# Performance work log

Measured on AMD Instinct MI355X. Metric: run time of the kernel, lower is better.

## Reference

```python
import jax, jax.numpy as jnp
import numpy as np

WS = 10                      # window radius
K = 2 * WS + 1               # 21
K2 = K * K                   # 441 window positions
SIG_COLOR = 1.0 / (0.1 * 0.1 * 2.0)
SIG_SPACE = 1.0 / (7.0 * 7.0 * 2.0)
LP = 0.8
C1 = 10.0
C2 = 5.0
ALPHA = 5.0
EPS = 1e-6


def _patches(img):
    """torch nn.Unfold(kernel_size=image_size, padding=WS) trick: returns the
    K2 zero-padded shifted copies of the image, shape (b, K2, c, h, w)."""
    b, c, h, w = img.shape
    p = jax.lax.conv_general_dilated_patches(img, (K, K), (1, 1), [(WS, WS), (WS, WS)])
    # (b, c*K2, h, w) with channel-major (c, ky, kx) ordering -> (b, K2, c, h, w)
    return p.reshape(b, c, K2, h, w).transpose(0, 2, 1, 3, 4)


def _edge_response(img):
    # local contrast: sum over window and channels of |I_j - I_i| (zero-padded
    # / non-positive neighbors masked out), shape (b, h, w)
    p = _patches(img)
    d = jnp.where(p > 0, p - img[:, None], 0.0)
    return jnp.abs(d).sum(axis=(1, 2))


def setup_inputs() -> dict:
    key = jax.random.key(0)
    k1, k2 = jax.random.split(key)
    original_images = jax.random.uniform(k1, (1, 3, 224, 224), dtype=jnp.float32)
    smooth_images = jax.random.uniform(k2, (1, 3, 224, 224), dtype=jnp.float32)
    return {"original_images": original_images, "smooth_images": smooth_images}


def reference(original_images, smooth_images):
    b, c, h, w = smooth_images.shape

    # ti_minus_tj: |T_j - T_i| with zero/non-positive padded neighbors zeroed;
    # the shifted copies are detached in the original (stop_gradient)
    sp = jax.lax.stop_gradient(_patches(smooth_images))
    ti = jnp.abs(jnp.where(sp > 0, sp - smooth_images[:, None], 0.0))  # (b,K2,c,h,w)

    # edge-response based region masks
    er_o = _edge_response(original_images)
    er_s = _edge_response(smooth_images)
    use_large = ((er_o < C1) & (er_s - er_o > C2))[:, None, None]  # (b,1,1,h,w)

    # spatial affinity ws (constant gaussian over window offsets)
    dy = jnp.arange(-WS, WS + 1)
    ws = jnp.exp(-SIG_SPACE * (dy[:, None] ** 2 + dy[None, :] ** 2).astype(jnp.float32))
    ws = ws.reshape(1, K2, 1, 1, 1)

    # color affinity wr from the guidance (original) image; note the original
    # code computes the affinity BEFORE masking the color difference, so the
    # affinity includes zero-padded neighbors -- replicated faithfully
    op = jax.lax.stop_gradient(_patches(original_images))
    cd = ((op - original_images[:, None]) ** 2).sum(axis=2, keepdims=True)  # (b,K2,1,h,w)
    wr = jnp.exp(-SIG_COLOR * cd)

    ws = jnp.where(use_large, ws, 0.0)
    wr = jnp.where(~use_large, wr, 0.0)

    scale = 1.0 / (h * w * b) / (WS * WS)  # note: window_size**2, not K2 (quirk kept)
    return scale * jnp.sum(ALPHA * ws * ti ** 2 + wr * (ti + EPS) ** LP)
```

## Files before the change

### kernel.cpp

```cpp
#include <hip/hip_runtime.h>


#define WSR 10
#define KK  21
#define HH  224
#define WW  224
#define HWSZ (HH*WW)
#define SIG_COLOR 50.0f
#define SIG_SPACE (1.0f/98.0f)
#define LPW 0.8f
#define C1T 10.0f
#define C2T 5.0f
#define ALPHA_W 5.0f
#define EPSV 1e-6f
#define LOG2E 1.44269504088896f

__device__ __forceinline__ float fexp2(float x) { return __builtin_amdgcn_exp2f(x); }
__device__ __forceinline__ float flog2(float x) { return __builtin_amdgcn_logf(x); }
__device__ __forceinline__ float fexpe(float x) { return fexp2(x * LOG2E); }

__global__ __launch_bounds__(256) void smooth_loss_main(
    const float* __restrict__ orig, const float* __restrict__ smo,
    float* __restrict__ partials)
{
    __shared__ float w1[KK];
    __shared__ float racc[4][256];

    const int tid = threadIdx.x;
    if (tid < KK) {
        float d = (float)(tid - WSR);
        w1[tid] = fexpe(-SIG_SPACE * d * d);
    }
    __syncthreads();

    const int lane = tid & 63;
    const int wv   = tid >> 6;
    const int pix  = blockIdx.x * 64 + lane;
    const int py   = pix / WW;
    const int px   = pix - py * WW;

    const float oc0 = orig[pix], oc1 = orig[pix + HWSZ], oc2 = orig[pix + 2*HWSZ];
    const float sc0 = smo[pix],  sc1 = smo[pix + HWSZ],  sc2 = smo[pix + 2*HWSZ];

    const int ky0 = (wv == 0) ? 0 : (5 * wv + 1);
    const int kyn = (wv == 0) ? 6 : 5;

    float er_o = 0.f, er_s = 0.f, sl = 0.f, ss = 0.f;

    for (int kyi = 0; kyi < kyn; ++kyi) {
        const int ky = ky0 + kyi;
        const int y  = py + ky - WSR;
        const bool yv = ((unsigned)y < (unsigned)HH);
        const float wy = w1[ky];
        const int rb = y * WW;
        #pragma unroll 7
        for (int kx = 0; kx < KK; ++kx) {
            const int x = px + kx - WSR;
            const bool v = yv & ((unsigned)x < (unsigned)WW);
            const int ni = rb + x;
            float o0 = 0.f, o1 = 0.f, o2 = 0.f;
            float s0 = 0.f, s1 = 0.f, s2 = 0.f;
            if (v) {
                o0 = orig[ni]; o1 = orig[ni + HWSZ]; o2 = orig[ni + 2*HWSZ];
                s0 = smo[ni];  s1 = smo[ni + HWSZ];  s2 = smo[ni + 2*HWSZ];
            }
            float d0 = (o0 > 0.f) ? (o0 - oc0) : 0.f;
            float d1 = (o1 > 0.f) ? (o1 - oc1) : 0.f;
            float d2 = (o2 > 0.f) ? (o2 - oc2) : 0.f;
            er_o += fabsf(d0) + fabsf(d1) + fabsf(d2);
            float t0 = (s0 > 0.f) ? fabsf(s0 - sc0) : 0.f;
            float t1 = (s1 > 0.f) ? fabsf(s1 - sc1) : 0.f;
            float t2 = (s2 > 0.f) ? fabsf(s2 - sc2) : 0.f;
            er_s += t0 + t1 + t2;
            float e0 = o0 - oc0, e1 = o1 - oc1, e2 = o2 - oc2;
            float wr = fexpe(-SIG_COLOR * (e0*e0 + e1*e1 + e2*e2));
            float wsp = wy * w1[kx];
            sl += wsp * (t0*t0 + t1*t1 + t2*t2);
            float p0 = fexp2(LPW * flog2(t0 + EPSV));
            float p1 = fexp2(LPW * flog2(t1 + EPSV));
            float p2 = fexp2(LPW * flog2(t2 + EPSV));
            ss += wr * (p0 + p1 + p2);
        }
    }

    racc[0][tid] = er_o; racc[1][tid] = er_s;
    racc[2][tid] = sl;   racc[3][tid] = ss;
    __syncthreads();

    if (wv == 0) {
        float eo = racc[0][lane] + racc[0][64+lane] + racc[0][128+lane] + racc[0][192+lane];
        float es = racc[1][lane] + racc[1][64+lane] + racc[1][128+lane] + racc[1][192+lane];
        float l  = racc[2][lane] + racc[2][64+lane] + racc[2][128+lane] + racc[2][192+lane];
        float s  = racc[3][lane] + racc[3][64+lane] + racc[3][128+lane] + racc[3][192+lane];
        const bool use_large = (eo < C1T) && ((es - eo) > C2T);
        float contrib = use_large ? (ALPHA_W * l) : s;
        #pragma unroll
        for (int off = 32; off > 0; off >>= 1)
            contrib += __shfl_down(contrib, off, 64);
        if (lane == 0) partials[blockIdx.x] = contrib;
    }
}

__global__ __launch_bounds__(256) void smooth_loss_reduce(
    const float* __restrict__ partials, float* __restrict__ out, int n)
{
    __shared__ float red[256];
    const int tid = threadIdx.x;
    float v = 0.f;
    for (int i = tid; i < n; i += 256) v += partials[i];
    red[tid] = v;
    __syncthreads();
    if (tid < 128) red[tid] += red[tid + 128];
    __syncthreads();
    if (tid < 64) {
        float x = red[tid] + red[tid + 64];
        #pragma unroll
        for (int off = 32; off > 0; off >>= 1)
            x += __shfl_down(x, off, 64);
        if (tid == 0)
            out[0] = x * (1.0f / ((float)HWSZ * (float)(WSR * WSR)));
    }
}

extern "C" void kernel_launch(void* const* d_in, const int* in_sizes, int n_in,
                              void* d_out, int out_size, void* d_ws, size_t ws_size,
                              hipStream_t stream) {
    const float* orig = (const float*)d_in[0];
    const float* smo  = (const float*)d_in[1];
    float* out = (float*)d_out;
    float* partials = (float*)d_ws;

    const int nblocks = (HWSZ / 64);
    smooth_loss_main<<<nblocks, 256, 0, stream>>>(orig, smo, partials);
    smooth_loss_reduce<<<1, 256, 0, stream>>>(partials, out, nblocks);
}
```

Baseline: 112.6 us.

## Stage halo tiles in LDS and fuse final reduction via last-block counter

Each block now loads a 2-row by 64-column tile of both images, plus a 10-pixel halo, into shared memory as packed float2 arrays. All window reads then come from LDS instead of repeated global or L1 loads. The separate reduce kernel is replaced by an atomic counter, so the last block to finish sums the partials, at the cost of a memset launch. The grid uses 4 column tiles of 64 over 224 columns, which wastes 32 lanes per row; those lanes are masked out of the sum.

Result: slower. 115.7 us (+2.7%).

```diff
diff --git a/kernel.cpp b/kernel.cpp
--- a/kernel.cpp
+++ b/kernel.cpp
@@ -15,110 +15,145 @@
 #define EPSV 1e-6f
 #define LOG2E 1.44269504088896f
 
+#define TX 64
+#define TY 2
+#define HALO_W (TX + 2*WSR)
+#define HALO_H (TY + 2*WSR)
+#define HSZ (HALO_W * HALO_H)
+#define NBX 4
+#define NBY (HH / TY)
+#define NBLK (NBX * NBY)
+
 __device__ __forceinline__ float fexp2(float x) { return __builtin_amdgcn_exp2f(x); }
 __device__ __forceinline__ float flog2(float x) { return __builtin_amdgcn_logf(x); }
-__device__ __forceinline__ float fexpe(float x) { return fexp2(x * LOG2E); }
 
-__global__ __launch_bounds__(256) void smooth_loss_main(
+__global__ __launch_bounds__(512) void smooth_loss_fused(
     const float* __restrict__ orig, const float* __restrict__ smo,
-    float* __restrict__ partials)
+    float* __restrict__ partials, unsigned* __restrict__ counter,
+    float* __restrict__ out)
 {
+    __shared__ float2 tA[HSZ];
+    __shared__ float2 tB[HSZ];
+    __shared__ float2 tC[HSZ];
     __shared__ float w1[KK];
-    __shared__ float racc[4][256];
+    __shared__ float racc0[512], racc1[512], racc2[512], racc3[512];
+    __shared__ float red[2];
+    __shared__ float red2[8];
+    __shared__ int lastflag;
 
     const int tid = threadIdx.x;
+    const int bid = blockIdx.x;
+    const int bx  = bid & (NBX - 1);
+    const int by  = bid >> 2;
+
     if (tid < KK) {
         float d = (float)(tid - WSR);
-        w1[tid] = fexpe(-SIG_SPACE * d * d);
+        w1[tid] = fexp2(-SIG_SPACE * LOG2E * d * d);
+    }
+
+    const int gx0 = bx * TX - WSR;
+    const int gy0 = by * TY - WSR;
+    for (int i = tid; i < HSZ; i += 512) {
+        int r = i / HALO_W;
+        int c = i - r * HALO_W;
+        int gy = gy0 + r, gx = gx0 + c;
+        bool v = ((unsigned)gy < (unsigned)HH) & ((unsigned)gx < (unsigned)WW);
+        int gi = gy * WW + gx;
+        float o0=0.f,o1=0.f,o2=0.f,s0=0.f,s1=0.f,s2=0.f;
+        if (v) {
+            o0 = orig[gi]; o1 = orig[gi+HWSZ]; o2 = orig[gi+2*HWSZ];
+            s0 = smo[gi];  s1 = smo[gi+HWSZ];  s2 = smo[gi+2*HWSZ];
+        }
+        tA[i] = make_float2(o0,o1);
+        tB[i] = make_float2(o2,s0);
+        tC[i] = make_float2(s1,s2);
     }
     __syncthreads();
 
     const int lane = tid & 63;
     const int wv   = tid >> 6;
-    const int pix  = blockIdx.x * 64 + lane;
-    const int py   = pix / WW;
-    const int px   = pix - py * WW;
+    const int prow = wv & 1;
+    const int kg   = wv >> 1;
 
-    const float oc0 = orig[pix], oc1 = orig[pix + HWSZ], oc2 = orig[pix + 2*HWSZ];
-    const float sc0 = smo[pix],  sc1 = smo[pix + HWSZ],  sc2 = smo[pix + 2*HWSZ];
+    const int cpos = (prow + WSR) * HALO_W + (lane + WSR);
+    const float2 cA = tA[cpos], cB = tB[cpos], cC = tC[cpos];
+    const float oc0=cA.x, oc1=cA.y, oc2=cB.x, sc0=cB.y, sc1=cC.x, sc2=cC.y;
 
-    const int ky0 = (wv == 0) ? 0 : (5 * wv + 1);
-    const int kyn = (wv == 0) ? 6 : 5;
+    float er_o=0.f, er_s=0.f, sl=0.f, ss=0.f;
 
-    float er_o = 0.f, er_s = 0.f, sl = 0.f, ss = 0.f;
-
-    for (int kyi = 0; kyi < kyn; ++kyi) {
-        const int ky = ky0 + kyi;
-        const int y  = py + ky - WSR;
-        const bool yv = ((unsigned)y < (unsigned)HH);
+    for (int ky = kg; ky < KK; ky += 4) {
         const float wy = w1[ky];
-        const int rb = y * WW;
-        #pragma unroll 7
+        const int rb = (prow + ky) * HALO_W + lane;
+        #pragma unroll
         for (int kx = 0; kx < KK; ++kx) {
-            const int x = px + kx - WSR;
-            const bool v = yv & ((unsigned)x < (unsigned)WW);
-            const int ni = rb + x;
-            float o0 = 0.f, o1 = 0.f, o2 = 0.f;
-            float s0 = 0.f, s1 = 0.f, s2 = 0.f;
-            if (v) {
-                o0 = orig[ni]; o1 = orig[ni + HWSZ]; o2 = orig[ni + 2*HWSZ];
-                s0 = smo[ni];  s1 = smo[ni + HWSZ];  s2 = smo[ni + 2*HWSZ];
-            }
-            float d0 = (o0 > 0.f) ? (o0 - oc0) : 0.f;
-            float d1 = (o1 > 0.f) ? (o1 - oc1) : 0.f;
-            float d2 = (o2 > 0.f) ? (o2 - oc2) : 0.f;
-            er_o += fabsf(d0) + fabsf(d1) + fabsf(d2);
-            float t0 = (s0 > 0.f) ? fabsf(s0 - sc0) : 0.f;
-            float t1 = (s1 > 0.f) ? fabsf(s1 - sc1) : 0.f;
-            float t2 = (s2 > 0.f) ? fabsf(s2 - sc2) : 0.f;
+            float2 A = tA[rb + kx];
+            float2 B = tB[rb + kx];
+            float2 C = tC[rb + kx];
+            float e0 = A.x - oc0, e1 = A.y - oc1, e2 = B.x - oc2;
+            float a0 = (A.x > 0.f) ? fabsf(e0) : 0.f;
+            float a1 = (A.y > 0.f) ? fabsf(e1) : 0.f;
+            float a2 = (B.x > 0.f) ? fabsf(e2) : 0.f;
+            er_o += a0 + a1 + a2;
+            float t0 = (B.y > 0.f) ? fabsf(B.y - sc0) : 0.f;
+            float t1 = (C.x > 0.f) ? fabsf(C.x - sc1) : 0.f;
+            float t2 = (C.y > 0.f) ? fabsf(C.y - sc2) : 0.f;
             er_s += t0 + t1 + t2;
-            float e0 = o0 - oc0, e1 = o1 - oc1, e2 = o2 - oc2;
-            float wr = fexpe(-SIG_COLOR * (e0*e0 + e1*e1 + e2*e2));
+            float cd = e0*e0 + e1*e1 + e2*e2;
+            float wr = fexp2(cd * (-SIG_COLOR * LOG2E));
             float wsp = wy * w1[kx];
-            sl += wsp * (t0*t0 + t1*t1 + t2*t2);
+            sl = fmaf(wsp, t0*t0 + t1*t1 + t2*t2, sl);
             float p0 = fexp2(LPW * flog2(t0 + EPSV));
             float p1 = fexp2(LPW * flog2(t1 + EPSV));
             float p2 = fexp2(LPW * flog2(t2 + EPSV));
-            ss += wr * (p0 + p1 + p2);
+            ss = fmaf(wr, p0 + p1 + p2, ss);
         }
     }
 
-    racc[0][tid] = er_o; racc[1][tid] = er_s;
-    racc[2][tid] = sl;   racc[3][tid] = ss;
+    racc0[tid]=er_o; racc1[tid]=er_s; racc2[tid]=sl; racc3[tid]=ss;
     __syncthreads();
 
-    if (wv == 0) {
-        float eo = racc[0][lane] + racc[0][64+lane] + racc[0][128+lane] + racc[0][192+lane];
-        float es = racc[1][lane] + racc[1][64+lane] + racc[1][128+lane] + racc[1][192+lane];
-        float l  = racc[2][lane] + racc[2][64+lane] + racc[2][128+lane] + racc[2][192+lane];
-        float s  = racc[3][lane] + racc[3][64+lane] + racc[3][128+lane] + racc[3][192+lane];
-        const bool use_large = (eo < C1T) && ((es - eo) > C2T);
+    if (tid < 128) {
+        float eo=0.f, es=0.f, l=0.f, s=0.f;
+        #pragma unroll
+        for (int k = 0; k < 4; ++k) {
+            int t2i = lane + 64 * (prow + 2*k);
+            eo += racc0[t2i]; es += racc1[t2i];
+            l  += racc2[t2i]; s  += racc3[t2i];
+        }
+        bool use_large = (eo < C1T) && ((es - eo) > C2T);
         float contrib = use_large ? (ALPHA_W * l) : s;
+        int px = bx * TX + lane;
+        if (px >= WW) contrib = 0.f;
         #pragma unroll
         for (int off = 32; off > 0; off >>= 1)
             contrib += __shfl_down(contrib, off, 64);
-        if (lane == 0) partials[blockIdx.x] = contrib;
+        if (lane == 0) red[wv] = contrib;
     }
-}
+    __syncthreads();
 
-__global__ __launch_bounds__(256) void smooth_loss_reduce(
-    const float* __restrict__ partials, float* __restrict__ out, int n)
-{
-    __shared__ float red[256];
-    const int tid = threadIdx.x;
-    float v = 0.f;
-    for (int i = tid; i < n; i += 256) v += partials[i];
-    red[tid] = v;
+    if (tid == 0) {
+        partials[bid] = red[0] + red[1];
+        __threadfence();
+        unsigned old = atomicAdd(counter, 1u);
+        lastflag = (old == (unsigned)(NBLK - 1)) ? 1 : 0;
+    }
     __syncthreads();
-    if (tid < 128) red[tid] += red[tid + 128];
-    __syncthreads();
-    if (tid < 64) {
-        float x = red[tid] + red[tid + 64];
+
+    if (lastflag) {
+        float v = 0.f;
+        for (int i = tid; i < NBLK; i += 512)
+            v += atomicAdd(&partials[i], 0.0f);
         #pragma unroll
         for (int off = 32; off > 0; off >>= 1)
-            x += __shfl_down(x, off, 64);
-        if (tid == 0)
-            out[0] = x * (1.0f / ((float)HWSZ * (float)(WSR * WSR)));
+            v += __shfl_down(v, off, 64);
+        if (lane == 0) red2[wv] = v;
+        __syncthreads();
+        if (tid == 0) {
+            float t = 0.f;
+            #pragma unroll
+            for (int k = 0; k < 8; ++k) t += red2[k];
+            out[0] = t * (1.0f / ((float)HWSZ * (float)(WSR * WSR)));
+        }
     }
 }
 
@@ -128,9 +163,10 @@
     const float* orig = (const float*)d_in[0];
     const float* smo  = (const float*)d_in[1];
     float* out = (float*)d_out;
-    float* partials = (float*)d_ws;
 
-    const int nblocks = (HWSZ / 64);
-    smooth_loss_main<<<nblocks, 256, 0, stream>>>(orig, smo, partials);
-    smooth_loss_reduce<<<1, 256, 0, stream>>>(partials, out, nblocks);
+    unsigned* counter = (unsigned*)d_ws;
+    float* partials   = (float*)((char*)d_ws + 256);
+
+    hipMemsetAsync(d_ws, 0, 4, stream);
+    smooth_loss_fused<<<NBLK, 512, 0, stream>>>(orig, smo, partials, counter, out);
 }
```
